# Kernel optimization log

Hardware: AMD Instinct MI355X
Metric: run time of the kernel (lower is better)

Reference implementation:

```python
import jax, jax.numpy as jnp
import numpy as np

NINPUTS = 16
WIDTH = 128
KSIZE = 21
SPP = 8
BS, CI, H, W = 2, 3, 192, 192
EPS = 1e-08


def _conv(x, w, b, padding):
    y = jax.lax.conv_general_dilated(
        x, w, window_strides=(1, 1), padding=padding,
        dimension_numbers=("NCHW", "OIHW", "NCHW"))
    return y + b[None, :, None, None]


def apply_kernels(kernel, radiance, ksize):
    """Per-pixel predicted-kernel conv: fused gather-multiply-reduce over taps.
    kernel: (bs, ksize^2, kh, kw), radiance: (bs, ci, h, w).
    Replicates torch apply_kernels (normalization='sum') without materializing
    the (bs, ci, kh, kw, ksize^2) unfold tile tensor."""
    bs, k2, kh, kw = kernel.shape
    _, ci, h, w = radiance.shape
    needed = kh + ksize - 1
    if needed > h:
        crop = (needed - h) // 2
        if crop > 0:
            kernel = kernel[:, :, crop:-crop, crop:-crop]
        kh, kw = kernel.shape[2], kernel.shape[3]
    else:
        crop = (h - needed) // 2
        if crop > 0:
            radiance = radiance[:, :, crop:-crop, crop:-crop]
    taps = jnp.arange(k2, dtype=jnp.int32)
    dy = taps // ksize
    dx = taps % ksize

    def body(acc, idx):
        patch = jax.lax.dynamic_slice(radiance, (0, 0, dy[idx], dx[idx]),
                                      (bs, ci, kh, kw))
        kv = jax.lax.dynamic_slice_in_dim(kernel, idx, 1, axis=1)  # (bs,1,kh,kw)
        return acc + kv * patch, None

    acc0 = jnp.zeros((bs, ci, kh, kw), radiance.dtype)
    weighted_sum, _ = jax.lax.scan(body, acc0, taps)
    kernel_sum = jnp.sum(kernel, axis=1, keepdims=True)  # (bs,1,kh,kw)
    return weighted_sum, kernel_sum


def setup_inputs() -> dict:
    key = jax.random.key(0)
    ks = jax.random.split(key, 10)
    s = 0.05
    inp = {
        "features": jax.random.normal(ks[0], (BS, SPP, NINPUTS, H, W), jnp.float32),
        "radiance": jax.random.uniform(ks[1], (BS, SPP, CI, H, W), jnp.float32),
        # recurrent conv processor (simplified main_processor): SAME 3x3 conv
        "w_rnn": jax.random.normal(ks[2], (WIDTH, NINPUTS + WIDTH, 3, 3), jnp.float32) * s,
        "b_rnn": jnp.zeros((WIDTH,), jnp.float32),
        "w_k1": jax.random.normal(ks[3], (WIDTH, WIDTH + NINPUTS, 3, 3), jnp.float32) * s,
        "b_k1": jnp.zeros((WIDTH,), jnp.float32),
        "w_k2": jax.random.normal(ks[4], (WIDTH, WIDTH, 3, 3), jnp.float32) * s,
        "b_k2": jnp.zeros((WIDTH,), jnp.float32),
        "w_k3": jax.random.normal(ks[5], (KSIZE * KSIZE, WIDTH, 3, 3), jnp.float32) * s,
        "b_k3": jnp.zeros((KSIZE * KSIZE,), jnp.float32),
    }
    return inp


def reference(features, radiance, w_rnn, b_rnn, w_k1, b_k1, w_k2, b_k2, w_k3, b_k3):
    bs, spp, ci, h, w = radiance.shape
    lrelu = lambda x: jax.nn.leaky_relu(x, 0.01)
    state = jnp.zeros((bs, WIDTH, h, w), features.dtype)
    unnorm = sumw = max_k = None
    for step in range(spp):
        f = features[:, step]  # (bs, ninputs, h, w)
        rnn = lrelu(_conv(jnp.concatenate([f, state], axis=1), w_rnn, b_rnn, "SAME"))
        state = rnn
        nf = jnp.concatenate([rnn, f], axis=1)  # (bs, width+ninputs, h, w)
        k = lrelu(_conv(nf, w_k1, b_k1, "VALID"))
        k = lrelu(_conv(k, w_k2, b_k2, "VALID"))
        k = _conv(k, w_k3, b_k3, "VALID")  # (bs, ksize^2, h-6, w-6), linear out
        # online-softmax (flash-attention-style) running max/exp rescale
        new_max = jnp.max(k.reshape(bs, -1), axis=1).reshape(bs, 1, 1, 1)
        if step == 0:
            max_k = new_max
        else:
            old_max = max_k
            max_k = jnp.maximum(old_max, new_max)
        kern = jnp.exp(k - max_k)
        ws, ksum = apply_kernels(kern, radiance[:, step], KSIZE)
        if step == 0:
            unnorm, sumw = ws, ksum
        else:
            scale = jnp.exp(old_max - max_k)
            unnorm = unnorm * scale + ws
            sumw = sumw * scale + ksum
    return unnorm / (sumw + EPS)
```

## Files before the change

kernel.cpp:

```cpp
#include <hip/hip_runtime.h>
#include <stdint.h>

typedef _Float16 half8 __attribute__((ext_vector_type(8)));
typedef _Float16 half4 __attribute__((ext_vector_type(4)));
typedef __attribute__((ext_vector_type(8))) short short8;
typedef __attribute__((ext_vector_type(4))) float f32x4;
typedef __attribute__((ext_vector_type(16))) float f32x16;

__device__ __forceinline__ unsigned encf(float x){
  uint32_t u = __float_as_uint(x);
  return (u & 0x80000000u) ? ~u : (u | 0x80000000u);
}
__device__ __forceinline__ float decf(unsigned u){
  uint32_t b = (u & 0x80000000u) ? (u & 0x7FFFFFFFu) : ~u;
  return __uint_as_float(b);
}
__device__ __forceinline__ void gload16(const void* g, void* l){
  __builtin_amdgcn_global_load_lds(
      (const __attribute__((address_space(1))) void*)g,
      (__attribute__((address_space(3))) void*)l, 16, 0, 0);
}

__global__ __launch_bounds__(256) void zero_u32(unsigned* __restrict__ p, int n){
  for (int i = blockIdx.x*256 + threadIdx.x; i < n; i += gridDim.x*256) p[i] = 0u;
}

__global__ __launch_bounds__(256) void pack_w(const float* __restrict__ w, _Float16* __restrict__ wp,
                                              int CO, int CI, int COP, int CINP){
  int idx = blockIdx.x*256 + threadIdx.x;
  int total = 9*COP*CINP;
  if (idx >= total) return;
  int ci = idx % CINP;
  int rest = idx / CINP;
  int co = rest % COP;
  int t  = rest / COP;
  float v = 0.f;
  if (co < CO && ci < CI) v = w[((size_t)co*CI + ci)*9 + t];
  int kc = ci >> 4, chl = ci & 15;
  wp[(((size_t)kc*9 + t)*(COP/32) + (co>>5))*512 + (co&31)*16 + chl] = (_Float16)v;
}

__global__ __launch_bounds__(256) void pack_bias(const float* __restrict__ b, float* __restrict__ bp, int n, int npad){
  int i = blockIdx.x*256 + threadIdx.x;
  if (i < npad) bp[i] = (i < n) ? b[i] : 0.f;
}

__global__ __launch_bounds__(256) void pack_feat(const float* __restrict__ f,
                                                 _Float16* __restrict__ rnn_b,
                                                 _Float16* __restrict__ k1_in,
                                                 unsigned fbstr, unsigned rbstr, unsigned kbstr){
  int p = blockIdx.x*256 + threadIdx.x;
  if (p >= 36864) return;
  int b = blockIdx.y;
  int y = p / 192, x = p % 192;
  const float* fb = f + (size_t)b*fbstr;
  _Float16* r = rnn_b + (size_t)b*rbstr + ((size_t)(y+1)*194 + (x+1))*144;
  _Float16* k = k1_in + (size_t)b*kbstr + (size_t)p*144;
  #pragma unroll
  for (int c = 0; c < 16; ++c){
    _Float16 v = (_Float16)fb[c*36864 + p];
    r[c] = v;
    k[128 + c] = v;
  }
}

template<int CINP, bool RELU, bool K3, bool DUAL, bool RS, int MINW>
__global__ __launch_bounds__(128, MINW) void conv3(
    const _Float16* __restrict__ X, int Wst, unsigned xbstr,
    const _Float16* __restrict__ Wp, int COP,
    const float* __restrict__ bias,
    _Float16* __restrict__ Y, int Wst_out, int DCP, unsigned ybstr,
    _Float16* __restrict__ Y2, unsigned y2str,
    unsigned* __restrict__ slot, int Ho, int Wo,
    int nco)
{
  constexpr int KC    = CINP/16;
  constexpr int NW    = K3 ? 4 : (RS ? 2 : 4);
  constexpr int BROWS = K3 ? 8 : 4;
  constexpr int SROWS = BROWS + 2;
  constexpr int ITEMS = SROWS*34*2;
  constexpr int NRND  = (ITEMS + 127)/128;
  __shared__ _Float16 lds[2][ITEMS*8];

  const int tid  = threadIdx.x;
  const int lane = tid & 63;
  const int wid  = tid >> 6;
  const int l31  = lane & 31;
  const int hsel = lane >> 5;
  const int xb   = blockIdx.x * 32;
  const int yb   = blockIdx.y * BROWS;
  const int co_blk = blockIdx.z % nco;
  const int b      = blockIdx.z / nco;

  const _Float16* Xb = X + (size_t)b * xbstr;
  const int NG = COP/32;
  const size_t wtap = (size_t)NG*512;
  const _Float16* wbase = Wp
      + ((size_t)((K3 || RS) ? (co_blk*2) : (co_blk*4 + wid*2)))*512 + l31*16 + hsel*8;

  uint32_t goff[NRND];
  #pragma unroll
  for (int k = 0; k < NRND; ++k){
    int item = k*128 + tid;
    if (item < ITEMS){
      int row  = item / 68;
      int rem  = item % 68;
      int col  = rem >> 1;
      int half = rem & 1;
      int pix  = (yb + row)*Wst + xb + col;
      goff[k] = (uint32_t)(((uint32_t)pix*CINP + half*8) * 2);
    } else goff[k] = 0;
  }

  auto stage = [&](int buf, int kc){
    const char* xp = (const char*)Xb + (size_t)kc*32;
    char* lb = (char*)&lds[buf][0];
    #pragma unroll
    for (int k = 0; k < NRND; ++k){
      if (k*128 + tid < ITEMS)
        gload16(xp + goff[k], lb + k*2048 + wid*1024);
    }
  };

  uint32_t boffe[NW];
  #pragma unroll
  for (int n = 0; n < NW; ++n){
    const int row = K3 ? (wid*4 + n) : (RS ? (wid*2 + n) : n);
    boffe[n] = (uint32_t)((row*34 + l31)*16 + hsel*8);
  }

  f32x16 acc[NW][2] = {};
  half8 wreg[3][2];
  #pragma unroll
  for (int s3 = 0; s3 < 3; ++s3)
    #pragma unroll
    for (int g = 0; g < 2; ++g)
      wreg[s3][g] = *reinterpret_cast<const half8*>(wbase + (size_t)s3*wtap + g*512);

  stage(0, 0);
  __syncthreads();
  for (int kc = 0; kc < KC; ++kc){
    if (kc + 1 < KC) stage((kc+1)&1, kc+1);
    const _Float16* wt = wbase + (size_t)(kc*9)*wtap;
    const _Float16* lb = &lds[kc&1][0];
    half8 breg[2][NW];
    #pragma unroll
    for (int n = 0; n < NW; ++n)
      breg[0][n] = *reinterpret_cast<const half8*>(lb + boffe[n]);
    #pragma unroll
    for (int t = 0; t < 9; ++t){
      const int cur = t & 1, nxt = cur ^ 1;
      if (t < 8){
        const int ky1 = (t+1)/3, kx1 = (t+1) - ky1*3;
        #pragma unroll
        for (int n = 0; n < NW; ++n)
          breg[nxt][n] = *reinterpret_cast<const half8*>(lb + boffe[n] + (ky1*34 + kx1)*16);
      }
      #pragma unroll
      for (int n = 0; n < NW; ++n)
        #pragma unroll
        for (int g = 0; g < 2; ++g)
          acc[n][g] = __builtin_amdgcn_mfma_f32_32x32x16_f16(
              wreg[t % 3][g], breg[cur][n], acc[n][g], 0, 0, 0);
      #pragma unroll
      for (int g = 0; g < 2; ++g)
        wreg[t % 3][g] = *reinterpret_cast<const half8*>(wt + (size_t)(t+3)*wtap + g*512);
    }
    if (kc + 1 < KC) __syncthreads();
  }

  const int x = xb + l31;
  float lmax = -3.0e38f;
  #pragma unroll
  for (int n = 0; n < NW; ++n){
    const int y = yb + (K3 ? (wid*4 + n) : (RS ? (wid*2 + n) : n));
    if (y < Ho && x < Wo){
      #pragma unroll
      for (int g = 0; g < 2; ++g){
        #pragma unroll
        for (int q = 0; q < 4; ++q){
          const int cb = ((K3 || RS) ? (co_blk*64 + g*32) : ((wid*2 + g)*32))
                         + 4*hsel + 8*q;
          f32x4 bs = *reinterpret_cast<const f32x4*>(bias + cb);
          float v[4];
          #pragma unroll
          for (int j = 0; j < 4; ++j){
            float tv = acc[n][g][q*4 + j] + bs[j];
            if (RELU) tv = tv > 0.f ? tv : 0.01f*tv;
            v[j] = tv;
          }
          if constexpr (!K3){
            half4 pk;
            #pragma unroll
            for (int j = 0; j < 4; ++j) pk[j] = (_Float16)v[j];
            *reinterpret_cast<half4*>(Y + (size_t)b*ybstr + ((size_t)y*Wst_out + x)*DCP + cb) = pk;
            if constexpr (DUAL)
              *reinterpret_cast<half4*>(Y2 + (size_t)b*y2str
                  + ((size_t)(y+1)*194 + (x+1))*144 + 16 + cb) = pk;
          } else {
            _Float16* yp = Y + (size_t)b*ybstr;
            #pragma unroll
            for (int j = 0; j < 4; ++j){
              if (cb + j < 441){
                yp[(size_t)(cb+j)*29584 + (size_t)y*172 + x] = (_Float16)v[j];
                lmax = fmaxf(lmax, v[j]);
              }
            }
          }
        }
      }
    }
  }
  if constexpr (K3){
    #pragma unroll
    for (int o = 32; o > 0; o >>= 1) lmax = fmaxf(lmax, __shfl_xor(lmax, o));
    if (lane == 0) atomicMax(slot + b, encf(lmax));
  }
}

__global__ void update_max(float* __restrict__ st, unsigned* __restrict__ slot, int step){
  int b = threadIdx.x;
  if (b < 2){
    float nm   = decf(slot[b]);
    float oldM = st[2*b];
    float M    = (step == 0) ? nm : fmaxf(oldM, nm);
    st[2*b+1] = (step == 0) ? 0.f : expf(oldM - M);
    st[2*b]   = M;
    slot[b] = 0u;
  }
}

__global__ __launch_bounds__(256) void apply_acc(
    const _Float16* __restrict__ k3out, const float* __restrict__ rad,
    const float* __restrict__ st,
    float* __restrict__ unnorm, float* __restrict__ sumw)
{
  const int tx = threadIdx.x & 63, ty = threadIdx.x >> 6;
  const int x = blockIdx.x*64 + tx;
  const int y = blockIdx.y*4 + ty;
  const int b = blockIdx.z;
  if (x >= 172 || y >= 172) return;
  const float M = st[2*b], scale = st[2*b+1];
  const _Float16* kp = k3out + (size_t)b*13046544 + (size_t)y*172 + x;
  const float* rb = rad + (size_t)b*884736;
  float a0 = 0.f, a1 = 0.f, a2 = 0.f, aw = 0.f;
  for (int dy = 0; dy < 21; ++dy){
    const float* r0 = rb + (size_t)(y+dy)*192 + x;
    #pragma unroll
    for (int dx = 0; dx < 21; ++dx){
      float w = __expf((float)kp[(size_t)(dy*21+dx)*29584] - M);
      aw += w;
      a0 += w * r0[dx];
      a1 += w * r0[36864 + dx];
      a2 += w * r0[73728 + dx];
    }
  }
  size_t p = (size_t)b*88752 + (size_t)y*172 + x;
  size_t ps = (size_t)b*29584 + (size_t)y*172 + x;
  unnorm[p]        = unnorm[p]*scale        + a0;
  unnorm[p+29584]  = unnorm[p+29584]*scale  + a1;
  unnorm[p+59168]  = unnorm[p+59168]*scale  + a2;
  sumw[ps]         = sumw[ps]*scale         + aw;
}

__global__ __launch_bounds__(256) void finalize_out(const float* __restrict__ unnorm,
                                                    const float* __restrict__ sumw,
                                                    float* __restrict__ out){
  int i = blockIdx.x*256 + threadIdx.x;
  int b = blockIdx.y;
  if (i >= 88752) return;
  int p = i % 29584;
  out[(size_t)b*88752 + i] = unnorm[(size_t)b*88752 + i] / (sumw[(size_t)b*29584 + p] + 1e-8f);
}

extern "C" void kernel_launch(void* const* d_in, const int* in_sizes, int n_in,
                              void* d_out, int out_size, void* d_ws, size_t ws_size,
                              hipStream_t stream) {
  const float* features = (const float*)d_in[0];
  const float* radiance = (const float*)d_in[1];
  const float* w_rnn = (const float*)d_in[2];
  const float* b_rnn = (const float*)d_in[3];
  const float* w_k1  = (const float*)d_in[4];
  const float* b_k1  = (const float*)d_in[5];
  const float* w_k2  = (const float*)d_in[6];
  const float* b_k2  = (const float*)d_in[7];
  const float* w_k3  = (const float*)d_in[8];
  const float* b_k3  = (const float*)d_in[9];
  float* out = (float*)d_out;

  char* ws = (char*)d_ws;
  size_t off = 0;
  auto alloc = [&](size_t bytes)->char*{
    char* p = ws + off;
    off = (off + bytes + 255) & ~(size_t)255;
    return p;
  };
  const size_t WSLACK = 98304;
  _Float16* wp_rnn   = (_Float16*)alloc((size_t)9*128*144*2 + WSLACK);
  _Float16* wp_k1    = (_Float16*)alloc((size_t)9*128*144*2 + WSLACK);
  _Float16* wp_k2    = (_Float16*)alloc((size_t)9*128*128*2 + WSLACK);
  _Float16* wp_k3    = (_Float16*)alloc((size_t)9*448*128*2 + WSLACK);
  float*    bias_k3p = (float*)   alloc((size_t)448*4);
  const unsigned RB  = 194u*194u*144u;
  const unsigned KB  = (192u*192u+64u)*144u;
  const unsigned K2B = (194u*190u+64u)*128u;
  const unsigned K3B = (194u*188u+64u)*128u;
  const unsigned KOB = 441u*29584u;
  _Float16* rnn_inA = (_Float16*)alloc((size_t)2*RB*2);
  _Float16* rnn_inB = (_Float16*)alloc((size_t)2*RB*2);
  _Float16* k1_in  = (_Float16*)alloc((size_t)2*KB*2);
  _Float16* k2_in  = (_Float16*)alloc((size_t)2*K2B*2);
  _Float16* k3_in  = (_Float16*)alloc((size_t)2*K3B*2);
  _Float16* k3_out = (_Float16*)alloc((size_t)2*KOB*2);
  float*    accz   = (float*)   alloc((size_t)236678*4);
  if (off > ws_size) return;

  float*    unnorm = accz;
  float*    sumw   = accz + 177504;
  float*    st     = accz + 236672;
  unsigned* slot   = (unsigned*)(accz + 236676);

  _Float16* rnn_buf[2] = { rnn_inA, rnn_inB };

  pack_w<<<(9*128*144+255)/256, 256, 0, stream>>>(w_rnn, wp_rnn, 128, 144, 128, 144);
  pack_w<<<(9*128*144+255)/256, 256, 0, stream>>>(w_k1,  wp_k1,  128, 144, 128, 144);
  pack_w<<<(9*128*128+255)/256, 256, 0, stream>>>(w_k2,  wp_k2,  128, 128, 128, 128);
  pack_w<<<(9*448*128+255)/256, 256, 0, stream>>>(w_k3,  wp_k3,  441, 128, 448, 128);
  pack_bias<<<2, 256, 0, stream>>>(b_k3, bias_k3p, 441, 448);

  zero_u32<<<2048, 256, 0, stream>>>((unsigned*)rnn_inA, (int)RB);
  zero_u32<<<2048, 256, 0, stream>>>((unsigned*)rnn_inB, (int)RB);
  zero_u32<<<925,  256, 0, stream>>>((unsigned*)accz, 236678);

  for (int s = 0; s < 8; ++s){
    const float* f   = features + (size_t)s*16*36864;
    const float* rad = radiance + (size_t)s*3*36864;
    _Float16* rcur = rnn_buf[s & 1];
    _Float16* rnxt = rnn_buf[(s + 1) & 1];
    pack_feat<<<dim3(144,2), 256, 0, stream>>>(f, rcur, k1_in,
                                               8u*16u*36864u, RB, KB);
    conv3<144,true ,false,true ,true ,3><<<dim3(6,48,4), 128, 0, stream>>>(
        rcur, 194, RB, wp_rnn, 128, b_rnn, k1_in, 192, 144, KB,
        rnxt, RB, nullptr, 192, 192, 2);
    conv3<144,true ,false,false,true ,3><<<dim3(6,45,4), 128, 0, stream>>>(
        k1_in + (size_t)(7*192 + 7)*144, 192, KB, wp_k1, 128, b_k1,
        k2_in + (size_t)(7*190 + 7)*128, 190, 128, K2B,
        nullptr, 0, nullptr, 178, 178, 2);
    conv3<128,true ,false,false,true ,3><<<dim3(6,44,4), 128, 0, stream>>>(
        k2_in + (size_t)(7*190 + 7)*128, 190, K2B, wp_k2, 128, b_k2,
        k3_in + (size_t)(7*188 + 7)*128, 188, 128, K3B,
        nullptr, 0, nullptr, 174, 174, 2);
    conv3<128,false,true ,false,false,2><<<dim3(6,22,14), 128, 0, stream>>>(
        k3_in + (size_t)(7*188 + 7)*128, 188, K3B, wp_k3, 448, bias_k3p,
        k3_out, 0, 0, KOB, nullptr, 0, slot, 172, 172, 7);
    update_max<<<1, 64, 0, stream>>>(st, slot, s);
    apply_acc<<<dim3(3,43,2), 256, 0, stream>>>(k3_out, rad, st, unnorm, sumw);
  }
  finalize_out<<<dim3(347,2), 256, 0, stream>>>(unnorm, sumw, out);
}
```

Before: 2.247 ms.

## Split apply_acc taps across warps and shrink K3 conv row tile

The per-pixel kernel application now gives each block a single output row and splits the 441 taps across four wavefront groups, then reduces the partial sums through shared memory. This quadruples the number of threads working on the exp-weighted gather to improve latency hiding and occupancy. The final K3 conv also drops its 8-row tile to the same 4-row tile as the other convs, doubling its grid. The cost is less reuse of each staged input tile and extra shared-memory reduction and synchronisation.

Measured after the change: 2.459 ms. 1.09x slower.

```diff
diff --git a/kernel.cpp b/kernel.cpp
--- a/kernel.cpp
+++ b/kernel.cpp
@@ -75,10 +75,8 @@
     int nco)
 {
   constexpr int KC    = CINP/16;
-  constexpr int NW    = K3 ? 4 : (RS ? 2 : 4);
-  constexpr int BROWS = K3 ? 8 : 4;
-  constexpr int SROWS = BROWS + 2;
-  constexpr int ITEMS = SROWS*34*2;
+  constexpr int NW    = (K3 || RS) ? 2 : 4;
+  constexpr int ITEMS = 6*34*2;
   constexpr int NRND  = (ITEMS + 127)/128;
   __shared__ _Float16 lds[2][ITEMS*8];
 
@@ -88,7 +86,7 @@
   const int l31  = lane & 31;
   const int hsel = lane >> 5;
   const int xb   = blockIdx.x * 32;
-  const int yb   = blockIdx.y * BROWS;
+  const int yb   = blockIdx.y * 4;
   const int co_blk = blockIdx.z % nco;
   const int b      = blockIdx.z / nco;
 
@@ -125,7 +123,7 @@
   uint32_t boffe[NW];
   #pragma unroll
   for (int n = 0; n < NW; ++n){
-    const int row = K3 ? (wid*4 + n) : (RS ? (wid*2 + n) : n);
+    const int row = (K3 || RS) ? (wid*2 + n) : n;
     boffe[n] = (uint32_t)((row*34 + l31)*16 + hsel*8);
   }
 
@@ -173,7 +171,7 @@
   float lmax = -3.0e38f;
   #pragma unroll
   for (int n = 0; n < NW; ++n){
-    const int y = yb + (K3 ? (wid*4 + n) : (RS ? (wid*2 + n) : n));
+    const int y = yb + ((K3 || RS) ? (wid*2 + n) : n);
     if (y < Ho && x < Wo){
       #pragma unroll
       for (int g = 0; g < 2; ++g){
@@ -235,32 +233,44 @@
     const float* __restrict__ st,
     float* __restrict__ unnorm, float* __restrict__ sumw)
 {
-  const int tx = threadIdx.x & 63, ty = threadIdx.x >> 6;
-  const int x = blockIdx.x*64 + tx;
-  const int y = blockIdx.y*4 + ty;
+  __shared__ float red[4][4][64];
+  const int px = threadIdx.x & 63;
+  const int tg = threadIdx.x >> 6;
+  const int x = blockIdx.x*64 + px;
+  const int y = blockIdx.y;
   const int b = blockIdx.z;
-  if (x >= 172 || y >= 172) return;
-  const float M = st[2*b], scale = st[2*b+1];
-  const _Float16* kp = k3out + (size_t)b*13046544 + (size_t)y*172 + x;
-  const float* rb = rad + (size_t)b*884736;
+  const bool active = (x < 172);
+  const float M = st[2*b];
   float a0 = 0.f, a1 = 0.f, a2 = 0.f, aw = 0.f;
-  for (int dy = 0; dy < 21; ++dy){
-    const float* r0 = rb + (size_t)(y+dy)*192 + x;
-    #pragma unroll
-    for (int dx = 0; dx < 21; ++dx){
-      float w = __expf((float)kp[(size_t)(dy*21+dx)*29584] - M);
+  if (active){
+    const _Float16* kp = k3out + (size_t)b*13046544 + (size_t)y*172 + x;
+    const float* rb = rad + (size_t)b*884736;
+    int dy = 0, dx = tg;
+    for (int t = tg; t < 441; t += 4){
+      float w = __expf((float)kp[(size_t)t*29584] - M);
       aw += w;
-      a0 += w * r0[dx];
-      a1 += w * r0[36864 + dx];
-      a2 += w * r0[73728 + dx];
+      const float* r0 = rb + (size_t)(y+dy)*192 + (x+dx);
+      a0 += w * r0[0];
+      a1 += w * r0[36864];
+      a2 += w * r0[73728];
+      dx += 4; if (dx >= 21){ dx -= 21; ++dy; }
     }
   }
-  size_t p = (size_t)b*88752 + (size_t)y*172 + x;
-  size_t ps = (size_t)b*29584 + (size_t)y*172 + x;
-  unnorm[p]        = unnorm[p]*scale        + a0;
-  unnorm[p+29584]  = unnorm[p+29584]*scale  + a1;
-  unnorm[p+59168]  = unnorm[p+59168]*scale  + a2;
-  sumw[ps]         = sumw[ps]*scale         + aw;
+  red[tg][0][px] = a0; red[tg][1][px] = a1; red[tg][2][px] = a2; red[tg][3][px] = aw;
+  __syncthreads();
+  if (tg == 0 && active){
+    a0 = red[0][0][px] + red[1][0][px] + red[2][0][px] + red[3][0][px];
+    a1 = red[0][1][px] + red[1][1][px] + red[2][1][px] + red[3][1][px];
+    a2 = red[0][2][px] + red[1][2][px] + red[2][2][px] + red[3][2][px];
+    aw = red[0][3][px] + red[1][3][px] + red[2][3][px] + red[3][3][px];
+    const float scale = st[2*b+1];
+    size_t p  = (size_t)b*88752 + (size_t)y*172 + x;
+    size_t ps = (size_t)b*29584 + (size_t)y*172 + x;
+    unnorm[p]        = unnorm[p]*scale        + a0;
+    unnorm[p+29584]  = unnorm[p+29584]*scale  + a1;
+    unnorm[p+59168]  = unnorm[p+59168]*scale  + a2;
+    sumw[ps]         = sumw[ps]*scale         + aw;
+  }
 }
 
 __global__ __launch_bounds__(256) void finalize_out(const float* __restrict__ unnorm,
@@ -350,11 +360,11 @@
         k2_in + (size_t)(7*190 + 7)*128, 190, K2B, wp_k2, 128, b_k2,
         k3_in + (size_t)(7*188 + 7)*128, 188, 128, K3B,
         nullptr, 0, nullptr, 174, 174, 2);
-    conv3<128,false,true ,false,false,2><<<dim3(6,22,14), 128, 0, stream>>>(
+    conv3<128,false,true ,false,false,2><<<dim3(6,43,14), 128, 0, stream>>>(
         k3_in + (size_t)(7*188 + 7)*128, 188, K3B, wp_k3, 448, bias_k3p,
         k3_out, 0, 0, KOB, nullptr, 0, slot, 172, 172, 7);
     update_max<<<1, 64, 0, stream>>>(st, slot, s);
-    apply_acc<<<dim3(3,43,2), 256, 0, stream>>>(k3_out, rad, st, unnorm, sumw);
+    apply_acc<<<dim3(3,172,2), 256, 0, stream>>>(k3_out, rad, st, unnorm, sumw);
   }
   finalize_out<<<dim3(347,2), 256, 0, stream>>>(unnorm, sumw, out);
 }
```
